# Kernel optimization log

Hardware: AMD Instinct MI355X
Metric: run time of the kernel (lower is better)

## Reference

```python
import jax, jax.numpy as jnp
import numpy as np
import math

B, T, D, H = 4, 2048, 1024, 16
DK = D // H  # 64


def setup_inputs() -> dict:
    key = jax.random.key(0)
    ks = jax.random.split(key, 9)
    s = 0.02
    return {
        "x": jax.random.normal(ks[0], (B, T, D), jnp.float32),
        "wq": jax.random.normal(ks[1], (H, DK, D), jnp.float32) * s,
        "bq": jax.random.normal(ks[2], (H, DK), jnp.float32) * s,
        "wk": jax.random.normal(ks[3], (H, DK, D), jnp.float32) * s,
        "bk": jax.random.normal(ks[4], (H, DK), jnp.float32) * s,
        "wv": jax.random.normal(ks[5], (H, DK, D), jnp.float32) * s,
        "bv": jax.random.normal(ks[6], (H, DK), jnp.float32) * s,
        "wo": jax.random.normal(ks[7], (D, D), jnp.float32) * s,
        "bo": jax.random.normal(ks[8], (D,), jnp.float32) * s,
    }


def reference(x, wq, bq, wk, bk, wv, bv, wo, bo):
    # per-head projections (torch Linear: y = x @ W.T + b), all heads batched
    q = jnp.einsum("btc,hdc->bhtd", x, wq) + bq[None, :, None, :]
    k = jnp.einsum("btc,hdc->bhtd", x, wk) + bk[None, :, None, :]
    v = jnp.einsum("btc,hdc->bhtd", x, wv) + bv[None, :, None, :]
    scores = jnp.einsum("bhtd,bhsd->bhts", q, k) / math.sqrt(DK)
    causal = jnp.tril(jnp.ones((T, T), dtype=bool))  # True = keep
    scores = jnp.where(causal[None, None], scores, -jnp.inf)
    sm = jax.nn.softmax(scores, axis=-1)
    att = jnp.einsum("bhts,bhsd->bhtd", sm, v)
    # concat heads (head 0 first) -> [B, T, D]
    yh = att.transpose(0, 2, 1, 3).reshape(B, T, D)
    return yh @ wo.T + bo
```

## Files before the change

kernel.cpp:

```cpp
#include <hip/hip_runtime.h>
#include <hip/hip_bf16.h>
#include <cstdint>
#include <cstddef>

#define B_  4
#define T_  2048
#define D_  1024
#define H_  16
#define DK_ 64
#define M_  (B_ * T_)
#define NT8 (D_ / 64)

typedef __attribute__((ext_vector_type(8))) short bf16x8;
typedef __attribute__((ext_vector_type(4))) float f32x4;

static __device__ __forceinline__ unsigned short f2bf(float f) {
    __hip_bfloat16 h = __float2bfloat16(f);
    unsigned short u;
    __builtin_memcpy(&u, &h, 2);
    return u;
}

static __device__ __forceinline__ unsigned int pk2bf(float a, float b) {
    __hip_bfloat162 h = __float22bfloat162_rn(make_float2(a, b));
    unsigned int u;
    __builtin_memcpy(&u, &h, 4);
    return u;
}

static __device__ __forceinline__ void gl2lds16(const void* g, void* l) {
    __builtin_amdgcn_global_load_lds(
        (const __attribute__((address_space(1))) unsigned int*)g,
        (__attribute__((address_space(3))) unsigned int*)l,
        16, 0, 0);
}

__global__ __launch_bounds__(256) void cvt_bf16(
    const float* __restrict__ x,  const float* __restrict__ wq,
    const float* __restrict__ wk, const float* __restrict__ wv,
    const float* __restrict__ wo, unsigned short* __restrict__ dst)
{
    const int idx = blockIdx.x * 256 + threadIdx.x;
    const float* src;
    int off;
    if (idx < 2097152) { src = x; off = idx; }
    else {
        const int r = (idx - 2097152) >> 18;
        off = (idx - 2097152) & 262143;
        src = (r == 0) ? wq : (r == 1) ? wk : (r == 2) ? wv : wo;
    }
    float4 v = ((const float4*)src)[off];
    ushort4 o;
    o.x = f2bf(v.x); o.y = f2bf(v.y); o.z = f2bf(v.z); o.w = f2bf(v.w);
    ((ushort4*)dst)[idx] = o;
}

__global__ __launch_bounds__(512, 2) void gemm8p(
    const unsigned short* __restrict__ Amat,
    const unsigned short* __restrict__ w0,
    const unsigned short* __restrict__ w1,
    const unsigned short* __restrict__ w2,
    const float* __restrict__ b0,
    const float* __restrict__ b1,
    const float* __restrict__ b2,
    unsigned short* __restrict__ outU,
    float* __restrict__ outF,
    const int mode)
{
    const int s   = blockIdx.x;
    const int xcd = s & 7;
    const int idx = s >> 3;
    const int mm  = idx & 3;
    const int ns  = idx >> 2;
    const int sel = (mode == 0) ? (ns >> 3) : 3;
    const int nn  = (mode == 0) ? (ns & 7) : ns;
    const int m0  = (xcd * 4 + mm) * 256;
    const int n0  = nn * 128;

    const unsigned short* Bmat = (sel == 0) ? w0 : (sel == 1) ? w1 : w2;
    const float* bias          = (sel == 0) ? b0 : (sel == 1) ? b1 : b2;
    const bool selV = (sel == 2);

    const int tid  = threadIdx.x;
    const int w    = tid >> 6;
    const int lane = tid & 63;
    const int l15  = lane & 15, g = lane >> 4;
    const int lane8 = lane * 8;
    const int wm8  = (w >> 2) * 8;
    const int wn2  = (w & 3) * 2;

    __shared__ __align__(16) unsigned short As[2][32][512];
    __shared__ __align__(16) unsigned short Bs[2][16][512];

    f32x4 acc[8][2];
#pragma unroll
    for (int i = 0; i < 8; ++i)
#pragma unroll
        for (int j = 0; j < 2; ++j) acc[i][j] = (f32x4){0.f, 0.f, 0.f, 0.f};

    const unsigned short* aP[4];
#pragma unroll
    for (int j = 0; j < 4; ++j)
        aP[j] = Amat + (size_t)(m0 + (w >> 1) * 16 + 64 * j + l15) * D_
                     + (w & 1) * 32 + g * 8;
    const unsigned short* bP[2];
#pragma unroll
    for (int jb = 0; jb < 2; ++jb)
        bP[jb] = Bmat + (size_t)(n0 + w * 16 + l15) * D_ + jb * 32 + g * 8;

#pragma unroll
    for (int j = 0; j < 4; ++j) gl2lds16(aP[j], &As[0][w + 8 * j][0]);
    gl2lds16(bP[0], &Bs[0][2 * w    ][0]);
    gl2lds16(bP[1], &Bs[0][2 * w + 1][0]);
    gl2lds16(aP[0] + 64, &As[1][w     ][0]);
    gl2lds16(aP[2] + 64, &As[1][w + 16][0]);
    gl2lds16(bP[0] + 64, &Bs[1][2 * w    ][0]);
    gl2lds16(bP[1] + 64, &Bs[1][2 * w + 1][0]);
    asm volatile("s_waitcnt vmcnt(4)" ::: "memory");
    __builtin_amdgcn_s_barrier();

    bf16x8 bfr[2][2];
    bf16x8 ap[4][2];

    for (int kt = 0; kt < NT8; ++kt) {
        const int cur = kt & 1;
        const int ko  = kt * 64;

#pragma unroll
        for (int nj = 0; nj < 2; ++nj)
#pragma unroll
            for (int ks = 0; ks < 2; ++ks)
                bfr[nj][ks] = *(const bf16x8*)&Bs[cur][(wn2 + nj) * 2 + ks][lane8];
#pragma unroll
        for (int mi = 0; mi < 4; ++mi)
#pragma unroll
            for (int ks = 0; ks < 2; ++ks)
                ap[mi][ks] = *(const bf16x8*)&As[cur][(wm8 + mi) * 2 + ks][lane8];
        if (kt + 1 < NT8) {
            gl2lds16(aP[1] + ko + 64, &As[cur ^ 1][w + 8 ][0]);
            gl2lds16(aP[3] + ko + 64, &As[cur ^ 1][w + 24][0]);
        }
        __builtin_amdgcn_s_barrier();
        asm volatile("s_waitcnt lgkmcnt(0)" ::: "memory");
        __builtin_amdgcn_s_setprio(1);
        if (!selV) {
#pragma unroll
            for (int mi = 0; mi < 4; ++mi)
#pragma unroll
                for (int nj = 0; nj < 2; ++nj) {
                    acc[mi][nj] = __builtin_amdgcn_mfma_f32_16x16x32_bf16(
                        bfr[nj][0], ap[mi][0], acc[mi][nj], 0, 0, 0);
                    acc[mi][nj] = __builtin_amdgcn_mfma_f32_16x16x32_bf16(
                        bfr[nj][1], ap[mi][1], acc[mi][nj], 0, 0, 0);
                }
        } else {
#pragma unroll
            for (int mi = 0; mi < 4; ++mi)
#pragma unroll
                for (int nj = 0; nj < 2; ++nj) {
                    acc[mi][nj] = __builtin_amdgcn_mfma_f32_16x16x32_bf16(
                        ap[mi][0], bfr[nj][0], acc[mi][nj], 0, 0, 0);
                    acc[mi][nj] = __builtin_amdgcn_mfma_f32_16x16x32_bf16(
                        ap[mi][1], bfr[nj][1], acc[mi][nj], 0, 0, 0);
                }
        }
        __builtin_amdgcn_s_setprio(0);
        __builtin_amdgcn_s_barrier();

#pragma unroll
        for (int mi = 0; mi < 4; ++mi)
#pragma unroll
            for (int ks = 0; ks < 2; ++ks)
                ap[mi][ks] = *(const bf16x8*)&As[cur][(wm8 + 4 + mi) * 2 + ks][lane8];
        if (kt + 2 < NT8) {
            gl2lds16(aP[0] + ko + 128, &As[cur][w     ][0]);
            gl2lds16(aP[2] + ko + 128, &As[cur][w + 16][0]);
            gl2lds16(bP[0] + ko + 128, &Bs[cur][2 * w    ][0]);
            gl2lds16(bP[1] + ko + 128, &Bs[cur][2 * w + 1][0]);
        }
        __builtin_amdgcn_s_barrier();
        asm volatile("s_waitcnt lgkmcnt(0)" ::: "memory");
        __builtin_amdgcn_s_setprio(1);
        if (!selV) {
#pragma unroll
            for (int mi = 0; mi < 4; ++mi)
#pragma unroll
                for (int nj = 0; nj < 2; ++nj) {
                    acc[4 + mi][nj] = __builtin_amdgcn_mfma_f32_16x16x32_bf16(
                        bfr[nj][0], ap[mi][0], acc[4 + mi][nj], 0, 0, 0);
                    acc[4 + mi][nj] = __builtin_amdgcn_mfma_f32_16x16x32_bf16(
                        bfr[nj][1], ap[mi][1], acc[4 + mi][nj], 0, 0, 0);
                }
        } else {
#pragma unroll
            for (int mi = 0; mi < 4; ++mi)
#pragma unroll
                for (int nj = 0; nj < 2; ++nj) {
                    acc[4 + mi][nj] = __builtin_amdgcn_mfma_f32_16x16x32_bf16(
                        ap[mi][0], bfr[nj][0], acc[4 + mi][nj], 0, 0, 0);
                    acc[4 + mi][nj] = __builtin_amdgcn_mfma_f32_16x16x32_bf16(
                        ap[mi][1], bfr[nj][1], acc[4 + mi][nj], 0, 0, 0);
                }
        }
        __builtin_amdgcn_s_setprio(0);
        if (kt < NT8 - 2)       asm volatile("s_waitcnt vmcnt(4)" ::: "memory");
        else if (kt == NT8 - 2) asm volatile("s_waitcnt vmcnt(0)" ::: "memory");
        __builtin_amdgcn_s_barrier();
    }

    const int mbase = m0 + (w >> 2) * 128;
    const int nbase = n0 + (w & 3) * 32;
    const size_t BTD = (size_t)B_ * T_ * D_;

    if (mode == 1) {
#pragma unroll
        for (int nj = 0; nj < 2; ++nj) {
            const int ch0 = nbase + nj * 16 + g * 4;
            const float4 bb = *(const float4*)(bias + ch0);
#pragma unroll
            for (int mi = 0; mi < 8; ++mi) {
                const int tok = mbase + mi * 16 + l15;
                float4 r;
                r.x = acc[mi][nj][0] + bb.x;
                r.y = acc[mi][nj][1] + bb.y;
                r.z = acc[mi][nj][2] + bb.z;
                r.w = acc[mi][nj][3] + bb.w;
                *(float4*)(outF + (size_t)tok * D_ + ch0) = r;
            }
        }
    } else if (!selV) {
        unsigned short* outp = outU + (size_t)sel * BTD;
        const float osc = (sel == 0) ? 0.125f * 1.44269504f : 1.0f;
#pragma unroll
        for (int nj = 0; nj < 2; ++nj) {
            const int ch0 = nbase + nj * 16 + g * 4;
            const int hh = ch0 >> 6, dk0 = ch0 & 63;
            const float4 bb = *(const float4*)(bias + ch0);
#pragma unroll
            for (int mi = 0; mi < 8; ++mi) {
                const int tok = mbase + mi * 16 + l15;
                const int b = tok >> 11, t = tok & (T_ - 1);
                ushort4 r;
                r.x = f2bf((acc[mi][nj][0] + bb.x) * osc);
                r.y = f2bf((acc[mi][nj][1] + bb.y) * osc);
                r.z = f2bf((acc[mi][nj][2] + bb.z) * osc);
                r.w = f2bf((acc[mi][nj][3] + bb.w) * osc);
                *(ushort4*)(outp + ((size_t)((b * H_ + hh) * T_ + t)) * DK_ + dk0) = r;
            }
        }
    } else {
        unsigned short* outp = outU + 2 * BTD;
#pragma unroll
        for (int nj = 0; nj < 2; ++nj) {
            const int ch = nbase + nj * 16 + l15;
            const int hh = ch >> 6, dk = ch & 63;
            const float bbv = bias[ch];
#pragma unroll
            for (int mi = 0; mi < 8; ++mi) {
                const int tok0 = mbase + mi * 16 + g * 4;
                const int b = tok0 >> 11, t0 = tok0 & (T_ - 1);
                ushort4 r;
                r.x = f2bf(acc[mi][nj][0] + bbv);
                r.y = f2bf(acc[mi][nj][1] + bbv);
                r.z = f2bf(acc[mi][nj][2] + bbv);
                r.w = f2bf(acc[mi][nj][3] + bbv);
                *(ushort4*)(outp + ((size_t)((b * H_ + hh) * DK_ + dk)) * T_ + t0) = r;
            }
        }
    }
}

__global__ __launch_bounds__(256) void attn(
    const unsigned short* __restrict__ qg, const unsigned short* __restrict__ kg,
    const unsigned short* __restrict__ vtg,
    unsigned short* __restrict__ yh)
{
    const int s    = blockIdx.x;
    const int xcd  = s & 7;
    const int t_   = s >> 3;
    const int bhl  = t_ >> 5;
    const int j    = t_ & 31;
    const int bh   = xcd * 8 + bhl;
    const int x    = 31 - j;
    const int h    = bh & (H_ - 1);
    const int b    = bh >> 4;
    const int tq0  = x * 64;
    const int nCh  = x + 1;

    const int tid  = threadIdx.x;
    const int w    = tid >> 6;
    const int lane = tid & 63;
    const int l15  = lane & 15;
    const int g    = lane >> 4;

    const size_t base = (size_t)bh * T_ * DK_;
    const unsigned short* Qb  = qg  + base;
    const unsigned short* Kb  = kg  + base;
    const unsigned short* Vtb = vtg + base;

    __shared__ __align__(16) unsigned short Kf[8][512];
    __shared__ __align__(16) unsigned short Vf[8][512];
    __shared__ __align__(16) unsigned short Pb[4][16][68];

    const int q0w = tq0 + w * 16;
    const int tq  = q0w + l15;

    bf16x8 qf0 = *(const bf16x8*)(Qb + (size_t)tq * DK_ + g * 8);
    bf16x8 qf1 = *(const bf16x8*)(Qb + (size_t)tq * DK_ + 32 + g * 8);

    bf16x8 ones;
#pragma unroll
    for (int jj = 0; jj < 8; ++jj) ones[jj] = (short)0x3F80;

    f32x4 o[4];
#pragma unroll
    for (int i = 0; i < 4; ++i) o[i] = (f32x4){0.f, 0.f, 0.f, 0.f};
    f32x4 lacc = {0.f, 0.f, 0.f, 0.f};

    const unsigned short* kSrc = Kb + (size_t)(w * 16 + l15) * DK_ + g * 8;
    const unsigned short* vSrc = Vtb + (size_t)(w * 16 + l15) * T_ + g * 8;

    bf16x8 kr0 = *(const bf16x8*)(kSrc);
    bf16x8 kr1 = *(const bf16x8*)(kSrc + 32);
    bf16x8 vr0 = *(const bf16x8*)(vSrc);
    bf16x8 vr1 = *(const bf16x8*)(vSrc + 32);

    for (int ch = 0; ch < nCh; ++ch) {
        const int s0 = ch * 64;
        __syncthreads();
        *(bf16x8*)&Kf[2 * w    ][lane * 8] = kr0;
        *(bf16x8*)&Kf[2 * w + 1][lane * 8] = kr1;
        *(bf16x8*)&Vf[2 * w    ][lane * 8] = vr0;
        *(bf16x8*)&Vf[2 * w + 1][lane * 8] = vr1;
        if (ch + 1 < nCh) {
            const size_t ko = (size_t)(ch + 1) * 64 * DK_;
            const int    vo = (ch + 1) * 64;
            kr0 = *(const bf16x8*)(kSrc + ko);
            kr1 = *(const bf16x8*)(kSrc + ko + 32);
            vr0 = *(const bf16x8*)(vSrc + vo);
            vr1 = *(const bf16x8*)(vSrc + vo + 32);
        }
        __syncthreads();

#pragma unroll
        for (int st = 0; st < 4; ++st) {
            const int sbase = s0 + st * 16;
            const bool live = (sbase <= q0w + 15);
            unsigned int pkl, pkh;
            if (live) {
                bf16x8 a0 = *(const bf16x8*)&Kf[st * 2 + 0][lane * 8];
                bf16x8 a1 = *(const bf16x8*)&Kf[st * 2 + 1][lane * 8];
                f32x4 sacc = {0.f, 0.f, 0.f, 0.f};
                sacc = __builtin_amdgcn_mfma_f32_16x16x32_bf16(a0, qf0, sacc, 0, 0, 0);
                sacc = __builtin_amdgcn_mfma_f32_16x16x32_bf16(a1, qf1, sacc, 0, 0, 0);
                float p0, p1, p2, p3;
                if (sbase + 15 > q0w) {
                    p0 = (sbase + g * 4 + 0 <= tq) ? exp2f(sacc[0]) : 0.f;
                    p1 = (sbase + g * 4 + 1 <= tq) ? exp2f(sacc[1]) : 0.f;
                    p2 = (sbase + g * 4 + 2 <= tq) ? exp2f(sacc[2]) : 0.f;
                    p3 = (sbase + g * 4 + 3 <= tq) ? exp2f(sacc[3]) : 0.f;
                } else {
                    p0 = exp2f(sacc[0]); p1 = exp2f(sacc[1]);
                    p2 = exp2f(sacc[2]); p3 = exp2f(sacc[3]);
                }
                pkl = pk2bf(p0, p1);
                pkh = pk2bf(p2, p3);
            } else {
                pkl = 0; pkh = 0;
            }
            uint2 pk; pk.x = pkl; pk.y = pkh;
            *(uint2*)&Pb[w][l15][st * 16 + g * 4] = pk;
        }

        bf16x8 pf0 = *(const bf16x8*)&Pb[w][l15][g * 8];
        bf16x8 pf1 = *(const bf16x8*)&Pb[w][l15][32 + g * 8];
        __builtin_amdgcn_s_setprio(1);
        lacc = __builtin_amdgcn_mfma_f32_16x16x32_bf16(ones, pf0, lacc, 0, 0, 0);
        lacc = __builtin_amdgcn_mfma_f32_16x16x32_bf16(ones, pf1, lacc, 0, 0, 0);
#pragma unroll
        for (int dt = 0; dt < 4; ++dt) {
            bf16x8 v0 = *(const bf16x8*)&Vf[dt * 2 + 0][lane * 8];
            bf16x8 v1 = *(const bf16x8*)&Vf[dt * 2 + 1][lane * 8];
            o[dt] = __builtin_amdgcn_mfma_f32_16x16x32_bf16(v0, pf0, o[dt], 0, 0, 0);
            o[dt] = __builtin_amdgcn_mfma_f32_16x16x32_bf16(v1, pf1, o[dt], 0, 0, 0);
        }
        __builtin_amdgcn_s_setprio(0);
    }

    const float inv = 1.f / lacc[0];
    unsigned short* yrow = yh + ((size_t)(b * T_ + tq)) * D_ + h * DK_;
#pragma unroll
    for (int dt = 0; dt < 4; ++dt) {
        ushort4 r;
        r.x = f2bf(o[dt][0] * inv); r.y = f2bf(o[dt][1] * inv);
        r.z = f2bf(o[dt][2] * inv); r.w = f2bf(o[dt][3] * inv);
        *(ushort4*)(yrow + dt * 16 + g * 4) = r;
    }
}

extern "C" void kernel_launch(void* const* d_in, const int* in_sizes, int n_in,
                              void* d_out, int out_size, void* d_ws, size_t ws_size,
                              hipStream_t stream) {
    const float* x  = (const float*)d_in[0];
    const float* wq = (const float*)d_in[1];
    const float* bq = (const float*)d_in[2];
    const float* wk = (const float*)d_in[3];
    const float* bk = (const float*)d_in[4];
    const float* wv = (const float*)d_in[5];
    const float* bv = (const float*)d_in[6];
    const float* wo = (const float*)d_in[7];
    const float* bo = (const float*)d_in[8];
    float* out = (float*)d_out;

    const size_t BTD = (size_t)B_ * T_ * D_;
    const size_t WSZ = (size_t)D_ * D_;
    unsigned short* xb  = (unsigned short*)d_ws;
    unsigned short* wqb = xb  + BTD;
    unsigned short* wkb = wqb + WSZ;
    unsigned short* wvb = wkb + WSZ;
    unsigned short* wob = wvb + WSZ;
    unsigned short* qb  = wob + WSZ;
    unsigned short* kb  = qb  + BTD;
    unsigned short* vtb = kb  + BTD;
    unsigned short* yhb = vtb + BTD;

    cvt_bf16<<<dim3(12288), 256, 0, stream>>>(x, wq, wk, wv, wo, xb);

    gemm8p<<<dim3(768), 512, 0, stream>>>(
        xb, wqb, wkb, wvb, bq, bk, bv, qb, (float*)nullptr, 0);

    attn<<<dim3(2048), 256, 0, stream>>>(qb, kb, vtb, yhb);

    gemm8p<<<dim3(256), 512, 0, stream>>>(
        yhb, wob, wob, wob, bo, bo, bo, (unsigned short*)nullptr, out, 1);
}
```

Baseline: 319.2 us.

## Double-buffer K/V tiles in LDS using direct global-to-LDS loads

Replaces the register-staged K/V prefetch in the attention kernel with direct global-to-LDS copies (gl2lds16) into a double-buffered LDS tile. The next chunk is loaded into the alternate buffer while the current one is consumed, and the two barriers per chunk become one. The aim is to cut VGPR pressure and LDS store instructions and to overlap loads with MFMA work, at the cost of doubling LDS use for K/V. Correctness depends on gl2lds16 completion being covered by the single barrier, since there is no explicit vmcnt wait.

```diff
diff --git a/kernel.cpp b/kernel.cpp
--- a/kernel.cpp
+++ b/kernel.cpp
@@ -298,8 +298,8 @@
     const unsigned short* Kb  = kg  + base;
     const unsigned short* Vtb = vtg + base;
 
-    __shared__ __align__(16) unsigned short Kf[8][512];
-    __shared__ __align__(16) unsigned short Vf[8][512];
+    __shared__ __align__(16) unsigned short Kf[2][8][512];
+    __shared__ __align__(16) unsigned short Vf[2][8][512];
     __shared__ __align__(16) unsigned short Pb[4][16][68];
 
     const int q0w = tq0 + w * 16;
@@ -317,30 +317,29 @@
     for (int i = 0; i < 4; ++i) o[i] = (f32x4){0.f, 0.f, 0.f, 0.f};
     f32x4 lacc = {0.f, 0.f, 0.f, 0.f};
 
-    const unsigned short* kSrc = Kb + (size_t)(w * 16 + l15) * DK_ + g * 8;
-    const unsigned short* vSrc = Vtb + (size_t)(w * 16 + l15) * T_ + g * 8;
-
-    bf16x8 kr0 = *(const bf16x8*)(kSrc);
-    bf16x8 kr1 = *(const bf16x8*)(kSrc + 32);
-    bf16x8 vr0 = *(const bf16x8*)(vSrc);
-    bf16x8 vr1 = *(const bf16x8*)(vSrc + 32);
+    const unsigned short* kP = Kb + (size_t)(w * 16 + l15) * DK_ + g * 8;
+    const unsigned short* vP = Vtb + (size_t)(w * 16 + l15) * T_ + g * 8;
+
+    gl2lds16(kP,      &Kf[0][2 * w    ][0]);
+    gl2lds16(kP + 32, &Kf[0][2 * w + 1][0]);
+    gl2lds16(vP,      &Vf[0][2 * w    ][0]);
+    gl2lds16(vP + 32, &Vf[0][2 * w + 1][0]);
+    const unsigned short* kN = kP + (size_t)64 * DK_;
+    const unsigned short* vN = vP + 64;
+    __syncthreads();
 
     for (int ch = 0; ch < nCh; ++ch) {
+        const int cur = ch & 1;
         const int s0 = ch * 64;
-        __syncthreads();
-        *(bf16x8*)&Kf[2 * w    ][lane * 8] = kr0;
-        *(bf16x8*)&Kf[2 * w + 1][lane * 8] = kr1;
-        *(bf16x8*)&Vf[2 * w    ][lane * 8] = vr0;
-        *(bf16x8*)&Vf[2 * w + 1][lane * 8] = vr1;
+
         if (ch + 1 < nCh) {
-            const size_t ko = (size_t)(ch + 1) * 64 * DK_;
-            const int    vo = (ch + 1) * 64;
-            kr0 = *(const bf16x8*)(kSrc + ko);
-            kr1 = *(const bf16x8*)(kSrc + ko + 32);
-            vr0 = *(const bf16x8*)(vSrc + vo);
-            vr1 = *(const bf16x8*)(vSrc + vo + 32);
-        }
-        __syncthreads();
+            gl2lds16(kN,      &Kf[cur ^ 1][2 * w    ][0]);
+            gl2lds16(kN + 32, &Kf[cur ^ 1][2 * w + 1][0]);
+            gl2lds16(vN,      &Vf[cur ^ 1][2 * w    ][0]);
+            gl2lds16(vN + 32, &Vf[cur ^ 1][2 * w + 1][0]);
+            kN += (size_t)64 * DK_;
+            vN += 64;
+        }
 
 #pragma unroll
         for (int st = 0; st < 4; ++st) {
@@ -348,8 +347,8 @@
             const bool live = (sbase <= q0w + 15);
             unsigned int pkl, pkh;
             if (live) {
-                bf16x8 a0 = *(const bf16x8*)&Kf[st * 2 + 0][lane * 8];
-                bf16x8 a1 = *(const bf16x8*)&Kf[st * 2 + 1][lane * 8];
+                bf16x8 a0 = *(const bf16x8*)&Kf[cur][st * 2 + 0][lane * 8];
+                bf16x8 a1 = *(const bf16x8*)&Kf[cur][st * 2 + 1][lane * 8];
                 f32x4 sacc = {0.f, 0.f, 0.f, 0.f};
                 sacc = __builtin_amdgcn_mfma_f32_16x16x32_bf16(a0, qf0, sacc, 0, 0, 0);
                 sacc = __builtin_amdgcn_mfma_f32_16x16x32_bf16(a1, qf1, sacc, 0, 0, 0);
@@ -379,12 +378,14 @@
         lacc = __builtin_amdgcn_mfma_f32_16x16x32_bf16(ones, pf1, lacc, 0, 0, 0);
 #pragma unroll
         for (int dt = 0; dt < 4; ++dt) {
-            bf16x8 v0 = *(const bf16x8*)&Vf[dt * 2 + 0][lane * 8];
-            bf16x8 v1 = *(const bf16x8*)&Vf[dt * 2 + 1][lane * 8];
+            bf16x8 v0 = *(const bf16x8*)&Vf[cur][dt * 2 + 0][lane * 8];
+            bf16x8 v1 = *(const bf16x8*)&Vf[cur][dt * 2 + 1][lane * 8];
             o[dt] = __builtin_amdgcn_mfma_f32_16x16x32_bf16(v0, pf0, o[dt], 0, 0, 0);
             o[dt] = __builtin_amdgcn_mfma_f32_16x16x32_bf16(v1, pf1, o[dt], 0, 0, 0);
         }
         __builtin_amdgcn_s_setprio(0);
+
+        __syncthreads();
     }
 
     const float inv = 1.f / lacc[0];
```

After: 333.1 us. 1.04x slower.

## Halve GEMM K-tile to 32 and raise occupancy to four blocks per CU

Applied to the files above, without the earlier changes.

The projection GEMM's K step shrinks from 64 to 32, so each double-buffered LDS stage is half the size. The A/B prefetch schedule is restructured into a simpler two-stage ring with one barrier pair per iteration, and launch bounds now request 4 blocks per CU instead of 2. The goal is more resident waves to hide memory latency. In exchange there are twice as many loop iterations and barriers, and register pressure rises under the tighter launch bound.

```diff
diff --git a/kernel.cpp b/kernel.cpp
--- a/kernel.cpp
+++ b/kernel.cpp
@@ -9,7 +9,7 @@
 #define H_  16
 #define DK_ 64
 #define M_  (B_ * T_)
-#define NT8 (D_ / 64)
+#define NT32 (D_ / 32)
 
 typedef __attribute__((ext_vector_type(8))) short bf16x8;
 typedef __attribute__((ext_vector_type(4))) float f32x4;
@@ -55,7 +55,7 @@
     ((ushort4*)dst)[idx] = o;
 }
 
-__global__ __launch_bounds__(512, 2) void gemm8p(
+__global__ __launch_bounds__(512, 4) void gemm8p(
     const unsigned short* __restrict__ Amat,
     const unsigned short* __restrict__ w0,
     const unsigned short* __restrict__ w1,
@@ -89,8 +89,8 @@
     const int wm8  = (w >> 2) * 8;
     const int wn2  = (w & 3) * 2;
 
-    __shared__ __align__(16) unsigned short As[2][32][512];
-    __shared__ __align__(16) unsigned short Bs[2][16][512];
+    __shared__ __align__(16) unsigned short As[2][16][512];
+    __shared__ __align__(16) unsigned short Bs[2][8][512];
 
     f32x4 acc[8][2];
 #pragma unroll
@@ -98,113 +98,62 @@
 #pragma unroll
         for (int j = 0; j < 2; ++j) acc[i][j] = (f32x4){0.f, 0.f, 0.f, 0.f};
 
-    const unsigned short* aP[4];
-#pragma unroll
-    for (int j = 0; j < 4; ++j)
-        aP[j] = Amat + (size_t)(m0 + (w >> 1) * 16 + 64 * j + l15) * D_
-                     + (w & 1) * 32 + g * 8;
-    const unsigned short* bP[2];
-#pragma unroll
-    for (int jb = 0; jb < 2; ++jb)
-        bP[jb] = Bmat + (size_t)(n0 + w * 16 + l15) * D_ + jb * 32 + g * 8;
-
-#pragma unroll
-    for (int j = 0; j < 4; ++j) gl2lds16(aP[j], &As[0][w + 8 * j][0]);
-    gl2lds16(bP[0], &Bs[0][2 * w    ][0]);
-    gl2lds16(bP[1], &Bs[0][2 * w + 1][0]);
-    gl2lds16(aP[0] + 64, &As[1][w     ][0]);
-    gl2lds16(aP[2] + 64, &As[1][w + 16][0]);
-    gl2lds16(bP[0] + 64, &Bs[1][2 * w    ][0]);
-    gl2lds16(bP[1] + 64, &Bs[1][2 * w + 1][0]);
-    asm volatile("s_waitcnt vmcnt(4)" ::: "memory");
+    const unsigned short* aP0 = Amat + (size_t)(m0 + w * 16 + l15) * D_ + g * 8;
+    const unsigned short* aP1 = Amat + (size_t)(m0 + (w + 8) * 16 + l15) * D_ + g * 8;
+    const unsigned short* bP  = Bmat + (size_t)(n0 + w * 16 + l15) * D_ + g * 8;
+
+    gl2lds16(aP0,      &As[0][w    ][0]);
+    gl2lds16(aP1,      &As[0][w + 8][0]);
+    gl2lds16(bP,       &Bs[0][w    ][0]);
+    gl2lds16(aP0 + 32, &As[1][w    ][0]);
+    gl2lds16(aP1 + 32, &As[1][w + 8][0]);
+    gl2lds16(bP + 32,  &Bs[1][w    ][0]);
+    asm volatile("s_waitcnt vmcnt(3)" ::: "memory");
     __builtin_amdgcn_s_barrier();
 
-    bf16x8 bfr[2][2];
-    bf16x8 ap[4][2];
-
-    for (int kt = 0; kt < NT8; ++kt) {
+    bf16x8 bfr[2];
+    bf16x8 ap[8];
+
+    for (int kt = 0; kt < NT32; ++kt) {
         const int cur = kt & 1;
-        const int ko  = kt * 64;
+        const int ko  = kt * 32;
 
 #pragma unroll
         for (int nj = 0; nj < 2; ++nj)
-#pragma unroll
-            for (int ks = 0; ks < 2; ++ks)
-                bfr[nj][ks] = *(const bf16x8*)&Bs[cur][(wn2 + nj) * 2 + ks][lane8];
-#pragma unroll
-        for (int mi = 0; mi < 4; ++mi)
-#pragma unroll
-            for (int ks = 0; ks < 2; ++ks)
-                ap[mi][ks] = *(const bf16x8*)&As[cur][(wm8 + mi) * 2 + ks][lane8];
-        if (kt + 1 < NT8) {
-            gl2lds16(aP[1] + ko + 64, &As[cur ^ 1][w + 8 ][0]);
-            gl2lds16(aP[3] + ko + 64, &As[cur ^ 1][w + 24][0]);
-        }
+            bfr[nj] = *(const bf16x8*)&Bs[cur][wn2 + nj][lane8];
+#pragma unroll
+        for (int mi = 0; mi < 8; ++mi)
+            ap[mi] = *(const bf16x8*)&As[cur][wm8 + mi][lane8];
+
         __builtin_amdgcn_s_barrier();
         asm volatile("s_waitcnt lgkmcnt(0)" ::: "memory");
+
+        if (kt + 2 < NT32) {
+            gl2lds16(aP0 + ko + 64, &As[cur][w    ][0]);
+            gl2lds16(aP1 + ko + 64, &As[cur][w + 8][0]);
+            gl2lds16(bP  + ko + 64, &Bs[cur][w    ][0]);
+        }
+
         __builtin_amdgcn_s_setprio(1);
         if (!selV) {
 #pragma unroll
-            for (int mi = 0; mi < 4; ++mi)
-#pragma unroll
-                for (int nj = 0; nj < 2; ++nj) {
+            for (int mi = 0; mi < 8; ++mi)
+#pragma unroll
+                for (int nj = 0; nj < 2; ++nj)
                     acc[mi][nj] = __builtin_amdgcn_mfma_f32_16x16x32_bf16(
-                        bfr[nj][0], ap[mi][0], acc[mi][nj], 0, 0, 0);
+                        bfr[nj], ap[mi], acc[mi][nj], 0, 0, 0);
+        } else {
+#pragma unroll
+            for (int mi = 0; mi < 8; ++mi)
+#pragma unroll
+                for (int nj = 0; nj < 2; ++nj)
                     acc[mi][nj] = __builtin_amdgcn_mfma_f32_16x16x32_bf16(
-                        bfr[nj][1], ap[mi][1], acc[mi][nj], 0, 0, 0);
-                }
-        } else {
-#pragma unroll
-            for (int mi = 0; mi < 4; ++mi)
-#pragma unroll
-                for (int nj = 0; nj < 2; ++nj) {
-                    acc[mi][nj] = __builtin_amdgcn_mfma_f32_16x16x32_bf16(
-                        ap[mi][0], bfr[nj][0], acc[mi][nj], 0, 0, 0);
-                    acc[mi][nj] = __builtin_amdgcn_mfma_f32_16x16x32_bf16(
-                        ap[mi][1], bfr[nj][1], acc[mi][nj], 0, 0, 0);
-                }
+                        ap[mi], bfr[nj], acc[mi][nj], 0, 0, 0);
         }
         __builtin_amdgcn_s_setprio(0);
-        __builtin_amdgcn_s_barrier();
-
-#pragma unroll
-        for (int mi = 0; mi < 4; ++mi)
-#pragma unroll
-            for (int ks = 0; ks < 2; ++ks)
-                ap[mi][ks] = *(const bf16x8*)&As[cur][(wm8 + 4 + mi) * 2 + ks][lane8];
-        if (kt + 2 < NT8) {
-            gl2lds16(aP[0] + ko + 128, &As[cur][w     ][0]);
-            gl2lds16(aP[2] + ko + 128, &As[cur][w + 16][0]);
-            gl2lds16(bP[0] + ko + 128, &Bs[cur][2 * w    ][0]);
-            gl2lds16(bP[1] + ko + 128, &Bs[cur][2 * w + 1][0]);
-        }
-        __builtin_amdgcn_s_barrier();
-        asm volatile("s_waitcnt lgkmcnt(0)" ::: "memory");
-        __builtin_amdgcn_s_setprio(1);
-        if (!selV) {
-#pragma unroll
-            for (int mi = 0; mi < 4; ++mi)
-#pragma unroll
-                for (int nj = 0; nj < 2; ++nj) {
-                    acc[4 + mi][nj] = __builtin_amdgcn_mfma_f32_16x16x32_bf16(
-                        bfr[nj][0], ap[mi][0], acc[4 + mi][nj], 0, 0, 0);
-                    acc[4 + mi][nj] = __builtin_amdgcn_mfma_f32_16x16x32_bf16(
-                        bfr[nj][1], ap[mi][1], acc[4 + mi][nj], 0, 0, 0);
-                }
-        } else {
-#pragma unroll
-            for (int mi = 0; mi < 4; ++mi)
-#pragma unroll
-                for (int nj = 0; nj < 2; ++nj) {
-                    acc[4 + mi][nj] = __builtin_amdgcn_mfma_f32_16x16x32_bf16(
-                        ap[mi][0], bfr[nj][0], acc[4 + mi][nj], 0, 0, 0);
-                    acc[4 + mi][nj] = __builtin_amdgcn_mfma_f32_16x16x32_bf16(
-                        ap[mi][1], bfr[nj][1], acc[4 + mi][nj], 0, 0, 0);
-                }
-        }
-        __builtin_amdgcn_s_setprio(0);
-        if (kt < NT8 - 2)       asm volatile("s_waitcnt vmcnt(4)" ::: "memory");
-        else if (kt == NT8 - 2) asm volatile("s_waitcnt vmcnt(0)" ::: "memory");
+
+        if (kt < NT32 - 2)       asm volatile("s_waitcnt vmcnt(3)" ::: "memory");
+        else if (kt == NT32 - 2) asm volatile("s_waitcnt vmcnt(0)" ::: "memory");
         __builtin_amdgcn_s_barrier();
     }
 
```

After: 1.171 ms. 267% more time.

## Fuse Q, K, V projections into one kernel sharing the x tile

Applied to the files above, without the earlier changes.

Replaces the generic 768-block QKV GEMM launch with a dedicated kernel. Each block of 512 threads loads one 128-row x tile and computes Q, K and V for the same 128 output columns, so the A operand is read from global memory once instead of three times. It runs a K-step of 32 with a double-buffered LDS pipeline and staggered prefetch of the K/V weight tiles. The epilogue writes Q (pre-scaled), K and transposed V. This holds three accumulator sets per thread, which raises register pressure and may cost occupancy.

```diff
diff --git a/kernel.cpp b/kernel.cpp
--- a/kernel.cpp
+++ b/kernel.cpp
@@ -10,6 +10,7 @@
 #define DK_ 64
 #define M_  (B_ * T_)
 #define NT8 (D_ / 64)
+#define NTF (D_ / 32)
 
 typedef __attribute__((ext_vector_type(8))) short bf16x8;
 typedef __attribute__((ext_vector_type(4))) float f32x4;
@@ -53,6 +54,160 @@
     ushort4 o;
     o.x = f2bf(v.x); o.y = f2bf(v.y); o.z = f2bf(v.z); o.w = f2bf(v.w);
     ((ushort4*)dst)[idx] = o;
+}
+
+__global__ __launch_bounds__(512, 2) void qkv_fused(
+    const unsigned short* __restrict__ xb,
+    const unsigned short* __restrict__ wqb,
+    const unsigned short* __restrict__ wkb,
+    const unsigned short* __restrict__ wvb,
+    const float* __restrict__ bq,
+    const float* __restrict__ bk,
+    const float* __restrict__ bv,
+    unsigned short* __restrict__ outU)
+{
+    const int s   = blockIdx.x;
+    const int xcd = s & 7;
+    const int idx = s >> 3;
+    const int mm  = idx & 7;
+    const int nn  = idx >> 3;
+    const int m0  = (xcd * 8 + mm) * 128;
+    const int n0  = nn * 128;
+
+    const int tid  = threadIdx.x;
+    const int w    = tid >> 6;
+    const int lane = tid & 63;
+    const int l15  = lane & 15, g = lane >> 4;
+    const int lane8 = lane * 8;
+    const int wm4  = (w >> 2) * 4;
+    const int wn2  = (w & 3) * 2;
+
+    __shared__ __align__(16) unsigned short As[2][8][512];
+    __shared__ __align__(16) unsigned short Bq[2][8][512];
+    __shared__ __align__(16) unsigned short Bk[2][8][512];
+    __shared__ __align__(16) unsigned short Bv[2][8][512];
+
+    f32x4 aq[4][2], ak[4][2], av[4][2];
+#pragma unroll
+    for (int i = 0; i < 4; ++i)
+#pragma unroll
+        for (int j = 0; j < 2; ++j) {
+            aq[i][j] = (f32x4){0.f, 0.f, 0.f, 0.f};
+            ak[i][j] = (f32x4){0.f, 0.f, 0.f, 0.f};
+            av[i][j] = (f32x4){0.f, 0.f, 0.f, 0.f};
+        }
+
+    const unsigned short* aP = xb  + (size_t)(m0 + w * 16 + l15) * D_ + g * 8;
+    const unsigned short* qP = wqb + (size_t)(n0 + w * 16 + l15) * D_ + g * 8;
+    const unsigned short* kP = wkb + (size_t)(n0 + w * 16 + l15) * D_ + g * 8;
+    const unsigned short* vP = wvb + (size_t)(n0 + w * 16 + l15) * D_ + g * 8;
+
+    gl2lds16(aP,      &As[0][w][0]);
+    gl2lds16(qP,      &Bq[0][w][0]);
+    gl2lds16(kP,      &Bk[0][w][0]);
+    gl2lds16(vP,      &Bv[0][w][0]);
+    gl2lds16(kP + 32, &Bk[1][w][0]);
+    gl2lds16(vP + 32, &Bv[1][w][0]);
+    asm volatile("s_waitcnt vmcnt(2)" ::: "memory");
+    __builtin_amdgcn_s_barrier();
+
+    bf16x8 ap[4], fq[2], fk[2], fv[2];
+
+    for (int kt = 0; kt < NTF; ++kt) {
+        const int cur = kt & 1;
+        const int ko  = kt * 32;
+
+#pragma unroll
+        for (int mi = 0; mi < 4; ++mi)
+            ap[mi] = *(const bf16x8*)&As[cur][wm4 + mi][lane8];
+#pragma unroll
+        for (int nj = 0; nj < 2; ++nj) {
+            fq[nj] = *(const bf16x8*)&Bq[cur][wn2 + nj][lane8];
+            fk[nj] = *(const bf16x8*)&Bk[cur][wn2 + nj][lane8];
+            fv[nj] = *(const bf16x8*)&Bv[cur][wn2 + nj][lane8];
+        }
+
+        if (kt + 1 < NTF) {
+            gl2lds16(aP + ko + 32, &As[cur ^ 1][w][0]);
+            gl2lds16(qP + ko + 32, &Bq[cur ^ 1][w][0]);
+        }
+
+        __builtin_amdgcn_s_barrier();
+        asm volatile("s_waitcnt lgkmcnt(0)" ::: "memory");
+
+        if (kt + 2 < NTF) {
+            gl2lds16(kP + ko + 64, &Bk[cur][w][0]);
+            gl2lds16(vP + ko + 64, &Bv[cur][w][0]);
+        }
+
+        __builtin_amdgcn_s_setprio(1);
+#pragma unroll
+        for (int mi = 0; mi < 4; ++mi)
+#pragma unroll
+            for (int nj = 0; nj < 2; ++nj) {
+                aq[mi][nj] = __builtin_amdgcn_mfma_f32_16x16x32_bf16(
+                    fq[nj], ap[mi], aq[mi][nj], 0, 0, 0);
+                ak[mi][nj] = __builtin_amdgcn_mfma_f32_16x16x32_bf16(
+                    fk[nj], ap[mi], ak[mi][nj], 0, 0, 0);
+                av[mi][nj] = __builtin_amdgcn_mfma_f32_16x16x32_bf16(
+                    ap[mi], fv[nj], av[mi][nj], 0, 0, 0);
+            }
+        __builtin_amdgcn_s_setprio(0);
+
+        if (kt < NTF - 2)       asm volatile("s_waitcnt vmcnt(2)" ::: "memory");
+        else if (kt == NTF - 2) asm volatile("s_waitcnt vmcnt(0)" ::: "memory");
+        __builtin_amdgcn_s_barrier();
+    }
+
+    const int mbase = m0 + (w >> 2) * 64;
+    const int nbase = n0 + (w & 3) * 32;
+    const size_t BTD = (size_t)B_ * T_ * D_;
+    const float osc = 0.125f * 1.44269504f;
+
+#pragma unroll
+    for (int nj = 0; nj < 2; ++nj) {
+        const int ch0 = nbase + nj * 16 + g * 4;
+        const int hh = ch0 >> 6, dk0 = ch0 & 63;
+        const float4 bbq = *(const float4*)(bq + ch0);
+        const float4 bbk = *(const float4*)(bk + ch0);
+#pragma unroll
+        for (int mi = 0; mi < 4; ++mi) {
+            const int tok = mbase + mi * 16 + l15;
+            const int b = tok >> 11, t = tok & (T_ - 1);
+            const size_t base = ((size_t)((b * H_ + hh) * T_ + t)) * DK_ + dk0;
+            ushort4 rq, rk;
+            rq.x = f2bf((aq[mi][nj][0] + bbq.x) * osc);
+            rq.y = f2bf((aq[mi][nj][1] + bbq.y) * osc);
+            rq.z = f2bf((aq[mi][nj][2] + bbq.z) * osc);
+            rq.w = f2bf((aq[mi][nj][3] + bbq.w) * osc);
+            rk.x = f2bf(ak[mi][nj][0] + bbk.x);
+            rk.y = f2bf(ak[mi][nj][1] + bbk.y);
+            rk.z = f2bf(ak[mi][nj][2] + bbk.z);
+            rk.w = f2bf(ak[mi][nj][3] + bbk.w);
+            *(ushort4*)(outU + base) = rq;
+            *(ushort4*)(outU + BTD + base) = rk;
+        }
+    }
+    {
+        unsigned short* outv = outU + 2 * BTD;
+#pragma unroll
+        for (int nj = 0; nj < 2; ++nj) {
+            const int ch = nbase + nj * 16 + l15;
+            const int hh = ch >> 6, dk = ch & 63;
+            const float bbv = bv[ch];
+#pragma unroll
+            for (int mi = 0; mi < 4; ++mi) {
+                const int tok0 = mbase + mi * 16 + g * 4;
+                const int b = tok0 >> 11, t0 = tok0 & (T_ - 1);
+                ushort4 r;
+                r.x = f2bf(av[mi][nj][0] + bbv);
+                r.y = f2bf(av[mi][nj][1] + bbv);
+                r.z = f2bf(av[mi][nj][2] + bbv);
+                r.w = f2bf(av[mi][nj][3] + bbv);
+                *(ushort4*)(outv + ((size_t)((b * H_ + hh) * DK_ + dk)) * T_ + t0) = r;
+            }
+        }
+    }
 }
 
 __global__ __launch_bounds__(512, 2) void gemm8p(
@@ -426,8 +581,8 @@
 
     cvt_bf16<<<dim3(12288), 256, 0, stream>>>(x, wq, wk, wv, wo, xb);
 
-    gemm8p<<<dim3(768), 512, 0, stream>>>(
-        xb, wqb, wkb, wvb, bq, bk, bv, qb, (float*)nullptr, 0);
+    qkv_fused<<<dim3(512), 512, 0, stream>>>(
+        xb, wqb, wkb, wvb, bq, bk, bv, qb);
 
     attn<<<dim3(2048), 256, 0, stream>>>(qb, kb, vtb, yhb);
 
```

After: 304.7 us. 4.5% less time.
